# Kernel tuning notes

Measured on AMD Instinct MI355X. Metric: run time of the kernel, lower is better.

Reference implementation:

```python
import jax, jax.numpy as jnp
import numpy as np

N, M, K, C, FF, H, OUT = 20000, 80000, 48, 64, 256, 4, 64


def _lin(x, w, b):
    return x @ w.T + b


def _bn(x, g, b, eps=1e-5):
    mu = x.mean(0)
    var = x.var(0)
    return (x - mu) * jax.lax.rsqrt(var + eps) * g + b


def setup_inputs() -> dict:
    key = jax.random.key(0)
    ks = jax.random.split(key, 24)
    voxel_features = jax.random.normal(ks[0], (M, C), jnp.float32)
    voxel_coords = jax.random.normal(ks[1], (M, 3), jnp.float32)
    query_coords = jax.random.normal(ks[2], (N, 3), jnp.float32)
    idx = jax.random.randint(ks[3], (N, K), 0, M)
    drop = jax.random.uniform(ks[4], (N, K)) < 0.1
    drop = drop.at[:, 0].set(False)  # keep >=1 valid key per query
    key_indices = jnp.where(drop, -1, idx)
    s = 0.05
    p = lambda i, shp: jax.random.normal(ks[i], shp, jnp.float32) * s
    return {
        "voxel_features": voxel_features,
        "voxel_coords": voxel_coords,
        "query_coords": query_coords,
        "key_indices": key_indices,
        "q_w": p(5, (C, 3)), "q_b": p(6, (C,)),
        "kpos_w": p(7, (C, 3)), "kpos_b": p(8, (C,)),
        "in_w": p(9, (3 * C, C)), "in_b": p(10, (3 * C,)),
        "out_w": p(11, (C, C)), "out_b": p(12, (C,)),
        "lin1_w": p(13, (FF, C)), "lin1_b": p(14, (FF,)),
        "lin2_w": p(15, (C, FF)), "lin2_b": p(16, (C,)),
        "norm_g": jnp.ones((C,), jnp.float32), "norm_b": jnp.zeros((C,), jnp.float32),
        "outl_w": p(17, (OUT, C)), "outl_b": p(18, (OUT,)),
        "obn_g": jnp.ones((OUT,), jnp.float32), "obn_b": jnp.zeros((OUT,), jnp.float32),
    }


def reference(voxel_features, voxel_coords, query_coords, key_indices,
              q_w, q_b, kpos_w, kpos_b, in_w, in_b, out_w, out_b,
              lin1_w, lin1_b, lin2_w, lin2_b, norm_g, norm_b,
              outl_w, outl_b, obn_g, obn_b):
    hd = C // H
    mask = key_indices < 0                      # (N,K) padded keys
    safe = jnp.where(mask, 0, key_indices)
    key_feats = voxel_features[safe]            # (N,K,C) hash-gather
    key_coords = voxel_coords[safe]             # (N,K,3)
    # query positional projection
    q_feat = jax.nn.relu(_lin(query_coords, q_w, q_b))          # (N,C)
    # relative coords + key positional conv1d(kernel=1) == linear on coord dim
    rel = key_coords - query_coords[:, None, :]                  # (N,K,3)
    key_feats = key_feats + jax.nn.relu(_lin(rel, kpos_w, kpos_b))
    # multihead attention, query length 1 per voxel
    Wq, Wk, Wv = jnp.split(in_w, 3, axis=0)
    bq, bk, bv = jnp.split(in_b, 3)
    q = (_lin(q_feat, Wq, bq) / jnp.sqrt(jnp.float32(hd))).reshape(N, H, hd)
    k = _lin(key_feats, Wk, bk).reshape(N, K, H, hd)
    v = _lin(key_feats, Wv, bv).reshape(N, K, H, hd)
    scores = jnp.einsum('nhd,nkhd->nhk', q, k)
    scores = jnp.where(mask[:, None, :], -jnp.inf, scores)
    attn = jax.nn.softmax(scores, axis=-1)
    ctx = jnp.einsum('nhk,nkhd->nhd', attn, v).reshape(N, C)
    att = _lin(ctx, out_w, out_b)                                # (N,C)
    # FFN + residual
    x = att + _lin(jax.nn.relu(_lin(att, lin1_w, lin1_b)), lin2_w, lin2_b)
    x = _bn(x, norm_g, norm_b)
    # output layer: Linear -> BN -> ReLU
    x = jax.nn.relu(_bn(_lin(x, outl_w, outl_b), obn_g, obn_b))
    return x
```

## Files before the change

kernel.cpp:

```cpp
#include <hip/hip_runtime.h>
#include <math.h>

#define N_Q 20000
#define KK 48
#define CC 64
#define FFD 256

#define TW_WOB   0
#define TW_WVT   4096
#define TW_L1B   8192
#define TW_L2B   16384
#define TW_OLB   24576
#define ST_OFF   32768
#define M_OFF    33024
#define VF_OFF   2593024
#define CTX_OFF  5153024

typedef short bf16x8 __attribute__((ext_vector_type(8)));
typedef float f32x4  __attribute__((ext_vector_type(4)));

__device__ __forceinline__ unsigned pk2(float a, float b) {
    unsigned r;
    asm("v_cvt_pk_bf16_f32 %0, %1, %2" : "=v"(r) : "v"(a), "v"(b));
    return r;
}
__device__ __forceinline__ unsigned f2bf(float a) {
    unsigned r;
    asm("v_cvt_pk_bf16_f32 %0, %1, 0" : "=v"(r) : "v"(a));
    return r & 0xffffu;
}
__device__ __forceinline__ float bflo(unsigned u) { return __uint_as_float(u << 16); }
__device__ __forceinline__ float bfhi(unsigned u) { return __uint_as_float(u & 0xffff0000u); }
__device__ __forceinline__ bf16x8 ldfrag(const unsigned short* p) {
    return *(const bf16x8*)p;
}
union U84 { unsigned u[4]; bf16x8 v; };

__global__ __launch_bounds__(256) void prep_m(
    const float* __restrict__ in_w, const float* __restrict__ out_w,
    const float* __restrict__ lin1_w, const float* __restrict__ lin2_w,
    const float* __restrict__ outl_w, const float* __restrict__ vfeat,
    const float* __restrict__ qcoord, const float* __restrict__ q_w,
    const float* __restrict__ q_b, const float* __restrict__ in_b,
    float* __restrict__ tw, unsigned short* __restrict__ vfeat_bf,
    float* __restrict__ stats, unsigned short* __restrict__ M_all)
{
    __shared__ __align__(16) unsigned short sQF[80*72];
    __shared__ __align__(16) unsigned short sQ[80*72];

    if (blockIdx.x >= 250) {
        int t = (blockIdx.x - 250) * 256 + threadIdx.x;
        unsigned* twu = (unsigned*)tw;
        if (t < 1280000) {
            float4 v = ((const float4*)vfeat)[t];
            uint2 p; p.x = pk2(v.x, v.y); p.y = pk2(v.z, v.w);
            ((uint2*)vfeat_bf)[t] = p;
        }
        if (t < 256) stats[t] = 0.0f;
        if (t < 4096) {
            if (t < 2048) {
                int p = t;
                int j2 = p & 3, lane = (p >> 2) & 63, nb = (p >> 8) & 3, ks = p >> 10;
                int nn = nb*16 + (lane & 15), k = ks*32 + (lane >> 4)*8 + 2*j2;
                twu[TW_WOB + p] = pk2(out_w[nn*64 + k], out_w[nn*64 + k + 1]);
            }
        } else if (t < 8192) {
            if (t < 6144) {
                int p = t - 4096;
                int j2 = p & 3, lane = (p >> 2) & 63, nb = (p >> 8) & 3, ks = p >> 10;
                int nn = nb*16 + (lane & 15), k = ks*32 + (lane >> 4)*8 + 2*j2;
                twu[TW_WVT + p] = pk2(in_w[(128 + nn)*64 + k], in_w[(128 + nn)*64 + k + 1]);
            }
        } else if (t < 16384) {
            int p = t - 8192;
            int j2 = p & 3, lane = (p >> 2) & 63, nb = (p >> 8) & 15, ks = p >> 12;
            int n = nb*16 + (lane & 15), k = ks*32 + (lane >> 4)*8 + 2*j2;
            twu[TW_L1B + p] = pk2(lin1_w[n*64 + k], lin1_w[n*64 + k + 1]);
        } else if (t < 24576) {
            int p = t - 16384;
            int j2 = p & 3, lane = (p >> 2) & 63, nb = (p >> 8) & 3, ks = p >> 10;
            int n = nb*16 + (lane & 15), k = ks*32 + (lane >> 4)*8 + 2*j2;
            twu[TW_L2B + p] = pk2(lin2_w[n*256 + k], lin2_w[n*256 + k + 1]);
        } else if (t < 26624) {
            int p = t - 24576;
            int j2 = p & 3, lane = (p >> 2) & 63, nb = (p >> 8) & 3, ks = p >> 10;
            int n = nb*16 + (lane & 15), k = ks*32 + (lane >> 4)*8 + 2*j2;
            twu[TW_OLB + p] = pk2(outl_w[n*64 + k], outl_w[n*64 + k + 1]);
        }
        return;
    }

    int t = threadIdx.x, base = blockIdx.x * 80;
    int colq = (t*4) & 63;
    float qwv[12];
    #pragma unroll
    for (int j = 0; j < 12; ++j) qwv[j] = q_w[colq*3 + j];
    float4 qb4 = *(const float4*)&q_b[colq];
    #pragma unroll
    for (int i = 0; i < 5; ++i) {
        int e = i*1024 + t*4, r = e >> 6, n = base + r;
        float c0 = qcoord[n*3], c1 = qcoord[n*3+1], c2 = qcoord[n*3+2];
        float f0 = fmaxf(fmaf(qwv[2],  c2, fmaf(qwv[1],  c1, fmaf(qwv[0], c0, qb4.x))), 0.f);
        float f1 = fmaxf(fmaf(qwv[5],  c2, fmaf(qwv[4],  c1, fmaf(qwv[3], c0, qb4.y))), 0.f);
        float f2 = fmaxf(fmaf(qwv[8],  c2, fmaf(qwv[7],  c1, fmaf(qwv[6], c0, qb4.z))), 0.f);
        float f3 = fmaxf(fmaf(qwv[11], c2, fmaf(qwv[10], c1, fmaf(qwv[9], c0, qb4.w))), 0.f);
        uint2 p; p.x = pk2(f0, f1); p.y = pk2(f2, f3);
        *(uint2*)&sQF[r*72 + colq] = p;
    }
    int w = t >> 6, lane = t & 63, l16 = lane & 15, quad = lane >> 4;
    bf16x8 qbf[2], kbf[4];
    {
        const float* qrow = in_w + (w*16 + l16)*64;
        #pragma unroll
        for (int ks = 0; ks < 2; ++ks) {
            float4 aa = *(const float4*)&qrow[ks*32 + quad*8];
            float4 bb = *(const float4*)&qrow[ks*32 + quad*8 + 4];
            U84 u;
            u.u[0] = pk2(aa.x, aa.y); u.u[1] = pk2(aa.z, aa.w);
            u.u[2] = pk2(bb.x, bb.y); u.u[3] = pk2(bb.z, bb.w);
            qbf[ks] = u.v;
        }
        #pragma unroll
        for (int nb = 0; nb < 4; ++nb) {
            U84 u;
            if (quad < 2) {
                int jj = nb*16 + l16;
                #pragma unroll
                for (int j2 = 0; j2 < 4; ++j2) {
                    int k = quad*8 + 2*j2;
                    u.u[j2] = pk2(in_w[(64 + w*16 + k)*64 + jj],
                                  in_w[(64 + w*16 + k + 1)*64 + jj]);
                }
            } else {
                u.u[0] = u.u[1] = u.u[2] = u.u[3] = 0;
            }
            kbf[nb] = u.v;
        }
    }
    __syncthreads();

    int cq = w*16 + l16;
    float bq = in_b[cq];
    #pragma unroll
    for (int mb = 0; mb < 5; ++mb) {
        bf16x8 a0 = ldfrag(&sQF[(mb*16 + l16)*72 + quad*8]);
        bf16x8 a1 = ldfrag(&sQF[(mb*16 + l16)*72 + 32 + quad*8]);
        f32x4 acc = {0.f, 0.f, 0.f, 0.f};
        acc = __builtin_amdgcn_mfma_f32_16x16x32_bf16(a0, qbf[0], acc, 0, 0, 0);
        acc = __builtin_amdgcn_mfma_f32_16x16x32_bf16(a1, qbf[1], acc, 0, 0, 0);
        #pragma unroll
        for (int reg = 0; reg < 4; ++reg) {
            int row = mb*16 + quad*4 + reg;
            sQ[row*72 + cq] = (unsigned short)f2bf((acc[reg] + bq) * 0.25f);
        }
    }
    #pragma unroll
    for (int mb = 0; mb < 5; ++mb) {
        bf16x8 a = {0,0,0,0,0,0,0,0};
        if (quad < 2) a = ldfrag(&sQ[(mb*16 + l16)*72 + w*16 + quad*8]);
        f32x4 acc[4];
        #pragma unroll
        for (int nb = 0; nb < 4; ++nb) {
            f32x4 z = {0.f, 0.f, 0.f, 0.f};
            acc[nb] = __builtin_amdgcn_mfma_f32_16x16x32_bf16(a, kbf[nb], z, 0, 0, 0);
        }
        #pragma unroll
        for (int nb = 0; nb < 4; ++nb)
            #pragma unroll
            for (int reg = 0; reg < 4; ++reg) {
                int r = base + mb*16 + quad*4 + reg, j = nb*16 + l16;
                M_all[(size_t)r*256 + w*64 + j] = (unsigned short)f2bf(acc[nb][reg]);
            }
    }
}

__global__ __launch_bounds__(256, 4) void attn_kernel(
    const unsigned short* __restrict__ vfeat_bf, const float* __restrict__ vcoord,
    const float* __restrict__ qcoord, const int* __restrict__ kidx,
    const float* __restrict__ kpos_w, const float* __restrict__ kpos_b,
    const float* __restrict__ in_b,
    const float* __restrict__ tw, const unsigned short* __restrict__ M_all,
    unsigned short* __restrict__ ctx_bf)
{
    __shared__ __align__(16) unsigned short skf2[4][KK*64];
    int wv = threadIdx.x >> 6, c = threadIdx.x & 63;
    int n = blockIdx.x * 4 + wv;
    unsigned short* skf = skf2[wv];
    int l16 = c & 15, quad = c >> 4;

    const unsigned short* Mrow = M_all + (size_t)n*256 + (l16 & 3)*64 + quad*8;
    bf16x8 mf0 = ldfrag(Mrow);
    bf16x8 mf1 = ldfrag(Mrow + 32);
    const unsigned* VBu = (const unsigned*)(tw + TW_WVT);
    bf16x8 wvf[2][4];
    #pragma unroll
    for (int ks = 0; ks < 2; ++ks)
        #pragma unroll
        for (int nb = 0; nb < 4; ++nb)
            wvf[ks][nb] = ldfrag((const unsigned short*)&VBu[((ks*4 + nb)*64 + c)*4]);

    float qc0 = qcoord[n*3+0], qc1 = qcoord[n*3+1], qc2 = qcoord[n*3+2];

    int kread = c < 48 ? c : 47;
    int idxv = kidx[(size_t)n*KK + kread];
    int sfe = idxv < 0 ? 0 : idxv;
    float rl0 = vcoord[sfe*3+0] - qc0;
    float rl1 = vcoord[sfe*3+1] - qc1;
    float rl2 = vcoord[sfe*3+2] - qc2;

    int o8 = c >> 3, jb8 = (c & 7) * 8;
    float w8[24], b8[8];
    #pragma unroll
    for (int q = 0; q < 6; ++q)
        *(float4*)&w8[q*4] = *(const float4*)(kpos_w + jb8*3 + q*4);
    *(float4*)&b8[0] = *(const float4*)(kpos_b + jb8);
    *(float4*)&b8[4] = *(const float4*)(kpos_b + jb8 + 4);

    uint4 fv[6];
    #pragma unroll
    for (int i = 0; i < 6; ++i) {
        int row = 8*i + o8;
        int si = __shfl(idxv, row);
        si = si < 0 ? 0 : si;
        fv[i] = *(const uint4*)(vfeat_bf + (size_t)si*64 + jb8);
    }
    #pragma unroll
    for (int i = 0; i < 6; ++i) {
        int row = 8*i + o8;
        float rr0 = __shfl(rl0, row), rr1 = __shfl(rl1, row), rr2 = __shfl(rl2, row);
        unsigned uu[4] = {fv[i].x, fv[i].y, fv[i].z, fv[i].w};
        unsigned pp[4];
        #pragma unroll
        for (int q2 = 0; q2 < 4; ++q2) {
            int k0 = 2*q2, k1 = 2*q2 + 1;
            float gl = bflo(uu[q2]), gh = bfhi(uu[q2]);
            gl += fmaxf(fmaf(w8[3*k0+2], rr2, fmaf(w8[3*k0+1], rr1, fmaf(w8[3*k0], rr0, b8[k0]))), 0.f);
            gh += fmaxf(fmaf(w8[3*k1+2], rr2, fmaf(w8[3*k1+1], rr1, fmaf(w8[3*k1], rr0, b8[k1]))), 0.f);
            pp[q2] = pk2(gl, gh);
        }
        uint4 st; st.x = pp[0]; st.y = pp[1]; st.z = pp[2]; st.w = pp[3];
        *(uint4*)&skf[row*64 + (jb8 ^ ((row & 7) << 3))] = st;
    }

    unsigned long long vm = __ballot(c < 48 && idxv >= 0);
    bf16x8 a0s[3], a1s[3];
    float S[3][4];
    #pragma unroll
    for (int mb = 0; mb < 3; ++mb) {
        int r0 = mb*16 + l16, sw = (l16 & 7) << 3;
        a0s[mb] = ldfrag(&skf[r0*64 + ((quad*8) ^ sw)]);
        a1s[mb] = ldfrag(&skf[r0*64 + ((32 + quad*8) ^ sw)]);
        f32x4 acc = {0.f, 0.f, 0.f, 0.f};
        acc = __builtin_amdgcn_mfma_f32_16x16x32_bf16(a0s[mb], mf0, acc, 0, 0, 0);
        acc = __builtin_amdgcn_mfma_f32_16x16x32_bf16(a1s[mb], mf1, acc, 0, 0, 0);
        #pragma unroll
        for (int r = 0; r < 4; ++r) {
            int kk = mb*16 + quad*4 + r;
            S[mb][r] = ((vm >> kk) & 1ull) ? acc[r] : -1e30f;
        }
    }

    float mx = S[0][0];
    #pragma unroll
    for (int mb = 0; mb < 3; ++mb)
        #pragma unroll
        for (int r = 0; r < 4; ++r) mx = fmaxf(mx, S[mb][r]);
    mx = fmaxf(mx, __shfl_xor(mx, 16));
    mx = fmaxf(mx, __shfl_xor(mx, 32));
    float p[3][4], es = 0.f;
    #pragma unroll
    for (int mb = 0; mb < 3; ++mb)
        #pragma unroll
        for (int r = 0; r < 4; ++r) { p[mb][r] = __expf(S[mb][r] - mx); es += p[mb][r]; }
    es += __shfl_xor(es, 16);
    es += __shfl_xor(es, 32);
    float rinv = 1.0f / es;
    #pragma unroll
    for (int mb = 0; mb < 3; ++mb)
        #pragma unroll
        for (int r = 0; r < 4; ++r) p[mb][r] *= rinv;

    float cacc0 = 0.f, cacc1 = 0.f, cacc2 = 0.f, cacc3 = 0.f;
    #pragma unroll
    for (int mb = 0; mb < 3; ++mb) {
        f32x4 av[4];
        #pragma unroll
        for (int nb = 0; nb < 4; ++nb) {
            f32x4 z = {0.f, 0.f, 0.f, 0.f};
            z = __builtin_amdgcn_mfma_f32_16x16x32_bf16(a0s[mb], wvf[0][nb], z, 0, 0, 0);
            av[nb] = __builtin_amdgcn_mfma_f32_16x16x32_bf16(a1s[mb], wvf[1][nb], z, 0, 0, 0);
        }
        #pragma unroll
        for (int r = 0; r < 4; ++r) {
            float pv = p[mb][r];
            float p0 = __shfl(pv, quad*16 + 0);
            float p1 = __shfl(pv, quad*16 + 1);
            float p2 = __shfl(pv, quad*16 + 2);
            float p3 = __shfl(pv, quad*16 + 3);
            cacc0 = fmaf(p0, av[0][r], cacc0);
            cacc1 = fmaf(p1, av[1][r], cacc1);
            cacc2 = fmaf(p2, av[2][r], cacc2);
            cacc3 = fmaf(p3, av[3][r], cacc3);
        }
    }
    cacc0 += __shfl_xor(cacc0, 16); cacc0 += __shfl_xor(cacc0, 32);
    cacc1 += __shfl_xor(cacc1, 16); cacc1 += __shfl_xor(cacc1, 32);
    cacc2 += __shfl_xor(cacc2, 16); cacc2 += __shfl_xor(cacc2, 32);
    cacc3 += __shfl_xor(cacc3, 16); cacc3 += __shfl_xor(cacc3, 32);
    float cv = quad == 0 ? cacc0 : quad == 1 ? cacc1 : quad == 2 ? cacc2 : cacc3;
    cv += in_b[128 + c];
    ctx_bf[(size_t)n*64 + c] = (unsigned short)f2bf(cv);
}

__global__ __launch_bounds__(256) void ffn_kernel(
    const float* __restrict__ tw, const float* __restrict__ out_b,
    const float* __restrict__ lin1_b, const float* __restrict__ lin2_b,
    const unsigned short* __restrict__ ctx_bf, float* __restrict__ y_out,
    float* __restrict__ sum1, float* __restrict__ sumsq1)
{
    __shared__ __align__(16) unsigned short sA[80*72];
    __shared__ __align__(16) unsigned short sH[80*264];
    int t = threadIdx.x, base = blockIdx.x * 80;
    int w = t >> 6, lane = t & 63, l16 = lane & 15, quad = lane >> 4;
    const unsigned* WOB = (const unsigned*)(tw + TW_WOB);
    const unsigned* L1B = (const unsigned*)(tw + TW_L1B);
    const unsigned* L2B = (const unsigned*)(tw + TW_L2B);
    bf16x8 wob[2], b1f[2][4], b2f[8];
    #pragma unroll
    for (int ks = 0; ks < 2; ++ks)
        wob[ks] = ldfrag((const unsigned short*)&WOB[((ks*4 + w)*64 + lane)*4]);
    #pragma unroll
    for (int ks = 0; ks < 2; ++ks)
        #pragma unroll
        for (int nb = 0; nb < 4; ++nb)
            b1f[ks][nb] = ldfrag((const unsigned short*)&L1B[((ks*16 + w*4 + nb)*64 + lane)*4]);
    #pragma unroll
    for (int ks = 0; ks < 8; ++ks)
        b2f[ks] = ldfrag((const unsigned short*)&L2B[((ks*4 + w)*64 + lane)*4]);

    int c = w*16 + l16;
    float ob = out_b[c];
    f32x4 attacc[5];
    #pragma unroll
    for (int mb = 0; mb < 5; ++mb) {
        const unsigned short* crow = ctx_bf + (size_t)(base + mb*16 + l16)*64;
        bf16x8 a0 = ldfrag(crow + quad*8);
        bf16x8 a1 = ldfrag(crow + 32 + quad*8);
        f32x4 acc = {0.f, 0.f, 0.f, 0.f};
        acc = __builtin_amdgcn_mfma_f32_16x16x32_bf16(a0, wob[0], acc, 0, 0, 0);
        acc = __builtin_amdgcn_mfma_f32_16x16x32_bf16(a1, wob[1], acc, 0, 0, 0);
        #pragma unroll
        for (int reg = 0; reg < 4; ++reg) {
            float av = acc[reg] + ob;
            attacc[mb][reg] = av;
            int row = mb*16 + quad*4 + reg;
            sA[row*72 + c] = (unsigned short)f2bf(av);
        }
    }
    __syncthreads();

    #pragma unroll
    for (int mb = 0; mb < 5; ++mb) {
        bf16x8 a0 = ldfrag(&sA[(mb*16 + l16)*72 + quad*8]);
        bf16x8 a1 = ldfrag(&sA[(mb*16 + l16)*72 + 32 + quad*8]);
        #pragma unroll
        for (int nb = 0; nb < 4; ++nb) {
            f32x4 acc = {0.f, 0.f, 0.f, 0.f};
            acc = __builtin_amdgcn_mfma_f32_16x16x32_bf16(a0, b1f[0][nb], acc, 0, 0, 0);
            acc = __builtin_amdgcn_mfma_f32_16x16x32_bf16(a1, b1f[1][nb], acc, 0, 0, 0);
            int f = w*64 + nb*16 + l16;
            float bias = lin1_b[f];
            #pragma unroll
            for (int reg = 0; reg < 4; ++reg) {
                int row = mb*16 + quad*4 + reg;
                sH[row*264 + f] = (unsigned short)f2bf(fmaxf(acc[reg] + bias, 0.0f));
            }
        }
    }
    __syncthreads();

    float lb2 = lin2_b[c];
    float s = 0.f, ss = 0.f;
    #pragma unroll
    for (int mb = 0; mb < 5; ++mb) {
        f32x4 acc = {0.f, 0.f, 0.f, 0.f};
        #pragma unroll
        for (int ks = 0; ks < 8; ++ks) {
            bf16x8 a = ldfrag(&sH[(mb*16 + l16)*264 + ks*32 + quad*8]);
            acc = __builtin_amdgcn_mfma_f32_16x16x32_bf16(a, b2f[ks], acc, 0, 0, 0);
        }
        #pragma unroll
        for (int reg = 0; reg < 4; ++reg) {
            int r = base + mb*16 + quad*4 + reg;
            float y = attacc[mb][reg] + lb2 + acc[reg];
            y_out[(size_t)r*64 + c] = y;
            s += y; ss = fmaf(y, y, ss);
        }
    }
    s  += __shfl_xor(s, 16);  s  += __shfl_xor(s, 32);
    ss += __shfl_xor(ss, 16); ss += __shfl_xor(ss, 32);
    if (lane < 16) {
        atomicAdd(&sum1[c], s);
        atomicAdd(&sumsq1[c], ss);
    }
}

__global__ __launch_bounds__(256) void linout_kernel(
    const float* __restrict__ tw, const float* __restrict__ outl_b,
    const float* __restrict__ norm_g, const float* __restrict__ norm_b,
    const float* __restrict__ sum1, const float* __restrict__ sumsq1,
    const float* __restrict__ y, float* __restrict__ z_out,
    float* __restrict__ sum2, float* __restrict__ sumsq2)
{
    __shared__ __align__(16) unsigned short sX[80*72];
    int t = threadIdx.x, base = blockIdx.x * 80;
    int colq = (t*4) & 63;
    const float invN = 1.0f / 20000.0f;
    float4 sm = *(const float4*)&sum1[colq];
    float4 sq = *(const float4*)&sumsq1[colq];
    float4 g  = *(const float4*)&norm_g[colq];
    float4 bb = *(const float4*)&norm_b[colq];
    float mu0 = sm.x*invN, mu1 = sm.y*invN, mu2 = sm.z*invN, mu3 = sm.w*invN;
    float a0 = g.x / sqrtf(fmaf(-mu0, mu0, sq.x*invN) + 1e-5f);
    float a1 = g.y / sqrtf(fmaf(-mu1, mu1, sq.y*invN) + 1e-5f);
    float a2 = g.z / sqrtf(fmaf(-mu2, mu2, sq.z*invN) + 1e-5f);
    float a3 = g.w / sqrtf(fmaf(-mu3, mu3, sq.w*invN) + 1e-5f);
    float b0 = fmaf(-mu0, a0, bb.x), b1 = fmaf(-mu1, a1, bb.y);
    float b2 = fmaf(-mu2, a2, bb.z), b3 = fmaf(-mu3, a3, bb.w);
    #pragma unroll
    for (int i = 0; i < 5; ++i) {
        int e = i*1024 + t*4, r = e >> 6;
        float4 v = *(const float4*)&y[(size_t)(base + r)*64 + colq];
        uint2 p;
        p.x = pk2(fmaf(v.x, a0, b0), fmaf(v.y, a1, b1));
        p.y = pk2(fmaf(v.z, a2, b2), fmaf(v.w, a3, b3));
        *(uint2*)&sX[r*72 + colq] = p;
    }
    int w = t >> 6, lane = t & 63, l16 = lane & 15, quad = lane >> 4;
    const unsigned* OLB = (const unsigned*)(tw + TW_OLB);
    bf16x8 obf[2];
    #pragma unroll
    for (int ks = 0; ks < 2; ++ks)
        obf[ks] = ldfrag((const unsigned short*)&OLB[((ks*4 + w)*64 + lane)*4]);
    __syncthreads();

    int co = w*16 + l16;
    float ob = outl_b[co];
    float s = 0.f, ss = 0.f;
    #pragma unroll
    for (int mb = 0; mb < 5; ++mb) {
        bf16x8 x0 = ldfrag(&sX[(mb*16 + l16)*72 + quad*8]);
        bf16x8 x1 = ldfrag(&sX[(mb*16 + l16)*72 + 32 + quad*8]);
        f32x4 acc = {0.f, 0.f, 0.f, 0.f};
        acc = __builtin_amdgcn_mfma_f32_16x16x32_bf16(x0, obf[0], acc, 0, 0, 0);
        acc = __builtin_amdgcn_mfma_f32_16x16x32_bf16(x1, obf[1], acc, 0, 0, 0);
        #pragma unroll
        for (int reg = 0; reg < 4; ++reg) {
            int r = base + mb*16 + quad*4 + reg;
            float zv = acc[reg] + ob;
            z_out[(size_t)r*64 + co] = zv;
            s += zv; ss = fmaf(zv, zv, ss);
        }
    }
    s  += __shfl_xor(s, 16);  s  += __shfl_xor(s, 32);
    ss += __shfl_xor(ss, 16); ss += __shfl_xor(ss, 32);
    if (lane < 16) {
        atomicAdd(&sum2[co], s);
        atomicAdd(&sumsq2[co], ss);
    }
}

__global__ void final_kernel(float* __restrict__ z,
    const float* __restrict__ sum2, const float* __restrict__ sumsq2,
    const float* __restrict__ obn_g, const float* __restrict__ obn_b)
{
    int i = blockIdx.x*blockDim.x + threadIdx.x;
    if (i >= N_Q*64/4) return;
    int o4 = (i*4) & 63;
    float4 sm = *(const float4*)&sum2[o4];
    float4 sq = *(const float4*)&sumsq2[o4];
    float4 g  = *(const float4*)&obn_g[o4];
    float4 b  = *(const float4*)&obn_b[o4];
    const float invN = 1.0f / 20000.0f;
    float mux = sm.x*invN, muy = sm.y*invN, muz = sm.z*invN, muw = sm.w*invN;
    float ax = g.x / sqrtf(fmaf(-mux, mux, sq.x*invN) + 1e-5f);
    float ay = g.y / sqrtf(fmaf(-muy, muy, sq.y*invN) + 1e-5f);
    float az = g.z / sqrtf(fmaf(-muz, muz, sq.z*invN) + 1e-5f);
    float aw = g.w / sqrtf(fmaf(-muw, muw, sq.w*invN) + 1e-5f);
    float4 v = ((float4*)z)[i];
    v.x = fmaxf(fmaf(v.x - mux, ax, b.x), 0.0f);
    v.y = fmaxf(fmaf(v.y - muy, ay, b.y), 0.0f);
    v.z = fmaxf(fmaf(v.z - muz, az, b.z), 0.0f);
    v.w = fmaxf(fmaf(v.w - muw, aw, b.w), 0.0f);
    ((float4*)z)[i] = v;
}

extern "C" void kernel_launch(void* const* d_in, const int* in_sizes, int n_in,
                              void* d_out, int out_size, void* d_ws, size_t ws_size,
                              hipStream_t stream)
{
    const float* vfeat  = (const float*)d_in[0];
    const float* vcoord = (const float*)d_in[1];
    const float* qcoord = (const float*)d_in[2];
    const int*   kidx   = (const int*)d_in[3];
    const float* q_w    = (const float*)d_in[4];
    const float* q_b    = (const float*)d_in[5];
    const float* kpos_w = (const float*)d_in[6];
    const float* kpos_b = (const float*)d_in[7];
    const float* in_w   = (const float*)d_in[8];
    const float* in_b   = (const float*)d_in[9];
    const float* out_w  = (const float*)d_in[10];
    const float* out_b  = (const float*)d_in[11];
    const float* lin1_w = (const float*)d_in[12];
    const float* lin1_b = (const float*)d_in[13];
    const float* lin2_w = (const float*)d_in[14];
    const float* lin2_b = (const float*)d_in[15];
    const float* norm_g = (const float*)d_in[16];
    const float* norm_b = (const float*)d_in[17];
    const float* outl_w = (const float*)d_in[18];
    const float* outl_b = (const float*)d_in[19];
    const float* obn_g  = (const float*)d_in[20];
    const float* obn_b  = (const float*)d_in[21];

    float* ws = (float*)d_ws;
    float* tw = ws;
    float* stats = ws + ST_OFF;
    float* sum1 = stats, *sumsq1 = stats + 64, *sum2 = stats + 128, *sumsq2 = stats + 192;
    unsigned short* M_all = (unsigned short*)(ws + M_OFF);
    unsigned short* vfeat_bf = (unsigned short*)(ws + VF_OFF);
    unsigned short* ctx_bf = (unsigned short*)(ws + CTX_OFF);
    float* xd = (float*)d_out;

    prep_m<<<5370, 256, 0, stream>>>(in_w, out_w, lin1_w, lin2_w, outl_w, vfeat,
                                     qcoord, q_w, q_b, in_b, tw, vfeat_bf,
                                     stats, M_all);
    attn_kernel<<<N_Q/4, 256, 0, stream>>>(vfeat_bf, vcoord, qcoord, kidx, kpos_w,
                                           kpos_b, in_b, tw, M_all, ctx_bf);
    ffn_kernel<<<250, 256, 0, stream>>>(tw, out_b, lin1_b, lin2_b, ctx_bf, xd,
                                        sum1, sumsq1);
    linout_kernel<<<250, 256, 0, stream>>>(tw, outl_b, norm_g, norm_b, sum1, sumsq1,
                                           xd, xd, sum2, sumsq2);
    final_kernel<<<1250, 256, 0, stream>>>(xd, sum2, sumsq2, obn_g, obn_b);
}
```

Measured before the change: 167.1 us.

## Process two queries per wavefront with overlapped gather of the second

The attention kernel now handles two queries per wavefront and launches half as many blocks. The second query's voxel-feature gather is issued before the first query's scores and context are computed, so gather latency overlaps with MFMA work. Per-wave setup (value-weight fragments, kpos weights, bias) is loaded once and amortised over two queries. The cost is higher register pressure (the min-blocks launch bound was dropped), which may lower occupancy.

```diff
diff --git a/kernel.cpp b/kernel.cpp
--- a/kernel.cpp
+++ b/kernel.cpp
@@ -174,56 +174,10 @@
     }
 }
 
-__global__ __launch_bounds__(256, 4) void attn_kernel(
-    const unsigned short* __restrict__ vfeat_bf, const float* __restrict__ vcoord,
-    const float* __restrict__ qcoord, const int* __restrict__ kidx,
-    const float* __restrict__ kpos_w, const float* __restrict__ kpos_b,
-    const float* __restrict__ in_b,
-    const float* __restrict__ tw, const unsigned short* __restrict__ M_all,
-    unsigned short* __restrict__ ctx_bf)
-{
-    __shared__ __align__(16) unsigned short skf2[4][KK*64];
-    int wv = threadIdx.x >> 6, c = threadIdx.x & 63;
-    int n = blockIdx.x * 4 + wv;
-    unsigned short* skf = skf2[wv];
-    int l16 = c & 15, quad = c >> 4;
-
-    const unsigned short* Mrow = M_all + (size_t)n*256 + (l16 & 3)*64 + quad*8;
-    bf16x8 mf0 = ldfrag(Mrow);
-    bf16x8 mf1 = ldfrag(Mrow + 32);
-    const unsigned* VBu = (const unsigned*)(tw + TW_WVT);
-    bf16x8 wvf[2][4];
-    #pragma unroll
-    for (int ks = 0; ks < 2; ++ks)
-        #pragma unroll
-        for (int nb = 0; nb < 4; ++nb)
-            wvf[ks][nb] = ldfrag((const unsigned short*)&VBu[((ks*4 + nb)*64 + c)*4]);
-
-    float qc0 = qcoord[n*3+0], qc1 = qcoord[n*3+1], qc2 = qcoord[n*3+2];
-
-    int kread = c < 48 ? c : 47;
-    int idxv = kidx[(size_t)n*KK + kread];
-    int sfe = idxv < 0 ? 0 : idxv;
-    float rl0 = vcoord[sfe*3+0] - qc0;
-    float rl1 = vcoord[sfe*3+1] - qc1;
-    float rl2 = vcoord[sfe*3+2] - qc2;
-
-    int o8 = c >> 3, jb8 = (c & 7) * 8;
-    float w8[24], b8[8];
-    #pragma unroll
-    for (int q = 0; q < 6; ++q)
-        *(float4*)&w8[q*4] = *(const float4*)(kpos_w + jb8*3 + q*4);
-    *(float4*)&b8[0] = *(const float4*)(kpos_b + jb8);
-    *(float4*)&b8[4] = *(const float4*)(kpos_b + jb8 + 4);
-
-    uint4 fv[6];
-    #pragma unroll
-    for (int i = 0; i < 6; ++i) {
-        int row = 8*i + o8;
-        int si = __shfl(idxv, row);
-        si = si < 0 ? 0 : si;
-        fv[i] = *(const uint4*)(vfeat_bf + (size_t)si*64 + jb8);
-    }
+__device__ __forceinline__ void consume_tile(unsigned short* skf, const uint4 fv[6],
+    int o8, int jb8, float rl0, float rl1, float rl2,
+    const float w8[24], const float b8[8])
+{
     #pragma unroll
     for (int i = 0; i < 6; ++i) {
         int row = 8*i + o8;
@@ -241,7 +195,12 @@
         uint4 st; st.x = pp[0]; st.y = pp[1]; st.z = pp[2]; st.w = pp[3];
         *(uint4*)&skf[row*64 + (jb8 ^ ((row & 7) << 3))] = st;
     }
-
+}
+
+__device__ __forceinline__ void score_ctx(const unsigned short* skf,
+    bf16x8 mf0, bf16x8 mf1, const bf16x8 wvf[2][4], float biasv,
+    int c, int l16, int quad, int idxv, unsigned short* ctx_row)
+{
     unsigned long long vm = __ballot(c < 48 && idxv >= 0);
     bf16x8 a0s[3], a1s[3];
     float S[3][4];
@@ -308,8 +267,84 @@
     cacc2 += __shfl_xor(cacc2, 16); cacc2 += __shfl_xor(cacc2, 32);
     cacc3 += __shfl_xor(cacc3, 16); cacc3 += __shfl_xor(cacc3, 32);
     float cv = quad == 0 ? cacc0 : quad == 1 ? cacc1 : quad == 2 ? cacc2 : cacc3;
-    cv += in_b[128 + c];
-    ctx_bf[(size_t)n*64 + c] = (unsigned short)f2bf(cv);
+    cv += biasv;
+    ctx_row[c] = (unsigned short)f2bf(cv);
+}
+
+__global__ __launch_bounds__(256) void attn_kernel(
+    const unsigned short* __restrict__ vfeat_bf, const float* __restrict__ vcoord,
+    const float* __restrict__ qcoord, const int* __restrict__ kidx,
+    const float* __restrict__ kpos_w, const float* __restrict__ kpos_b,
+    const float* __restrict__ in_b,
+    const float* __restrict__ tw, const unsigned short* __restrict__ M_all,
+    unsigned short* __restrict__ ctx_bf)
+{
+    __shared__ __align__(16) unsigned short skf2[4][KK*64];
+    int wv = threadIdx.x >> 6, c = threadIdx.x & 63;
+    int n0 = blockIdx.x * 8 + wv * 2;
+    unsigned short* skf = skf2[wv];
+    int l16 = c & 15, quad = c >> 4;
+    int o8 = c >> 3, jb8 = (c & 7) * 8;
+
+    const unsigned short* Mrow0 = M_all + (size_t)n0*256 + (l16 & 3)*64 + quad*8;
+    bf16x8 mf0a = ldfrag(Mrow0);
+    bf16x8 mf1a = ldfrag(Mrow0 + 32);
+    bf16x8 mf0b = ldfrag(Mrow0 + 256);
+    bf16x8 mf1b = ldfrag(Mrow0 + 288);
+
+    const unsigned* VBu = (const unsigned*)(tw + TW_WVT);
+    bf16x8 wvf[2][4];
+    #pragma unroll
+    for (int ks = 0; ks < 2; ++ks)
+        #pragma unroll
+        for (int nb = 0; nb < 4; ++nb)
+            wvf[ks][nb] = ldfrag((const unsigned short*)&VBu[((ks*4 + nb)*64 + c)*4]);
+
+    float qa0 = qcoord[n0*3+0], qa1 = qcoord[n0*3+1], qa2 = qcoord[n0*3+2];
+    float qb0 = qcoord[n0*3+3], qb1 = qcoord[n0*3+4], qb2 = qcoord[n0*3+5];
+    int kread = c < 48 ? c : 47;
+    int idx0 = kidx[(size_t)n0*KK + kread];
+    int idx1 = kidx[(size_t)(n0+1)*KK + kread];
+    int s0 = idx0 < 0 ? 0 : idx0;
+    int s1 = idx1 < 0 ? 0 : idx1;
+    float r00 = vcoord[s0*3+0] - qa0, r01 = vcoord[s0*3+1] - qa1, r02 = vcoord[s0*3+2] - qa2;
+    float r10 = vcoord[s1*3+0] - qb0, r11 = vcoord[s1*3+1] - qb1, r12 = vcoord[s1*3+2] - qb2;
+
+    float w8[24], b8[8];
+    #pragma unroll
+    for (int q = 0; q < 6; ++q)
+        *(float4*)&w8[q*4] = *(const float4*)(kpos_w + jb8*3 + q*4);
+    *(float4*)&b8[0] = *(const float4*)(kpos_b + jb8);
+    *(float4*)&b8[4] = *(const float4*)(kpos_b + jb8 + 4);
+
+    float biasv = in_b[128 + c];
+
+    uint4 fv[6];
+    #pragma unroll
+    for (int i = 0; i < 6; ++i) {
+        int row = 8*i + o8;
+        int si = __shfl(idx0, row);
+        si = si < 0 ? 0 : si;
+        fv[i] = *(const uint4*)(vfeat_bf + (size_t)si*64 + jb8);
+    }
+    consume_tile(skf, fv, o8, jb8, r00, r01, r02, w8, b8);
+
+    uint4 fv2[6];
+    #pragma unroll
+    for (int i = 0; i < 6; ++i) {
+        int row = 8*i + o8;
+        int si = __shfl(idx1, row);
+        si = si < 0 ? 0 : si;
+        fv2[i] = *(const uint4*)(vfeat_bf + (size_t)si*64 + jb8);
+    }
+
+    score_ctx(skf, mf0a, mf1a, wvf, biasv, c, l16, quad, idx0,
+              ctx_bf + (size_t)n0*64);
+
+    consume_tile(skf, fv2, o8, jb8, r10, r11, r12, w8, b8);
+
+    score_ctx(skf, mf0b, mf1b, wvf, biasv, c, l16, quad, idx1,
+              ctx_bf + (size_t)(n0+1)*64);
 }
 
 __global__ __launch_bounds__(256) void ffn_kernel(
@@ -534,7 +569,7 @@
     prep_m<<<5370, 256, 0, stream>>>(in_w, out_w, lin1_w, lin2_w, outl_w, vfeat,
                                      qcoord, q_w, q_b, in_b, tw, vfeat_bf,
                                      stats, M_all);
-    attn_kernel<<<N_Q/4, 256, 0, stream>>>(vfeat_bf, vcoord, qcoord, kidx, kpos_w,
+    attn_kernel<<<N_Q/8, 256, 0, stream>>>(vfeat_bf, vcoord, qcoord, kidx, kpos_w,
                                            kpos_b, in_b, tw, M_all, ctx_bf);
     ffn_kernel<<<250, 256, 0, stream>>>(tw, out_b, lin1_b, lin2_b, ctx_bf, xd,
                                         sum1, sumsq1);
```

Result: slower. 184.1 us (+10.2%).
